# Kernel optimization log

Hardware: AMD Instinct MI355X
Metric: run time of the kernel (lower is better)

The kernel has to match this reference:

```python
import jax, jax.numpy as jnp
import numpy as np

B, L, D, H, M = 2, 4096, 1024, 16, 256
DH = D // H
EPS = 1e-6
LN_EPS = 1e-5


def setup_inputs() -> dict:
    key = jax.random.key(0)
    ks = jax.random.split(key, 6)
    inp = {
        "x": jax.random.normal(ks[0], (B, L, D), jnp.float32),
        "Wq": jax.random.normal(ks[1], (D, D), jnp.float32) * (D ** -0.5),
        "Wk": jax.random.normal(ks[2], (D, D), jnp.float32) * (D ** -0.5),
        "Wv": jax.random.normal(ks[3], (D, D), jnp.float32) * (D ** -0.5),
        "Wo": jax.random.normal(ks[4], (D, D), jnp.float32) * (D ** -0.5),
        "proj": jax.random.normal(ks[5], (H, M, DH), jnp.float32),
        "ln_g": jnp.ones((D,), jnp.float32),
        "ln_b": jnp.zeros((D,), jnp.float32),
        "scale_factor": 2,
    }
    return inp


def _heads(t, W):
    b, l, _ = t.shape
    return (t @ W).reshape(b, l, H, DH).transpose(0, 2, 1, 3)  # bhld


def _favor_features(u, proj):
    # u: [B,H,L,DH] already scaled by d_head**-0.25; proj: [H,M,DH]
    dash = jnp.einsum("bhld,hmd->bhlm", u, proj)
    diag = 0.5 * jnp.sum(u * u, axis=-1, keepdims=True)  # [B,H,L,1]
    stab = jnp.max(dash, axis=-1, keepdims=True)
    return jnp.exp(dash - diag - stab) * (M ** -0.5)  # [B,H,L,M]


def reference(x, Wq, Wk, Wv, Wo, proj, ln_g, ln_b, scale_factor):
    b, l, d = x.shape
    # nearest-neighbor upsample along sequence (F.interpolate default mode)
    up = jnp.repeat(x, scale_factor, axis=1)  # [B, L*s, D]

    scale = DH ** -0.25
    q = _heads(up, Wq) * scale   # [B,H,Lq,DH]
    k = _heads(x, Wk) * scale    # [B,H,L,DH]
    v = _heads(x, Wv)            # [B,H,L,DH]

    qf = _favor_features(q, proj)  # [B,H,Lq,M]
    kf = _favor_features(k, proj)  # [B,H,L,M]

    kv = jnp.einsum("bhlm,bhld->bhmd", kf, v)          # [B,H,M,DH]
    k_sum = jnp.sum(kf, axis=2)                          # [B,H,M]
    z = 1.0 / (jnp.einsum("bhlm,bhm->bhl", qf, k_sum) + EPS)
    attn = jnp.einsum("bhlm,bhmd->bhld", qf, kv) * z[..., None]

    lq = attn.shape[2]
    y = attn.transpose(0, 2, 1, 3).reshape(b, lq, d) @ Wo
    y = jax.nn.gelu(y, approximate=False)

    mu = jnp.mean(y, axis=-1, keepdims=True)
    var = jnp.mean((y - mu) ** 2, axis=-1, keepdims=True)
    return (y - mu) * jax.lax.rsqrt(var + LN_EPS) * ln_g + ln_b
```

## Files before the change

### kernel.cpp

```cpp
#include <hip/hip_runtime.h>

static constexpr int kB  = 2;
static constexpr int kL  = 4096;
static constexpr int kD  = 1024;
static constexpr int kH  = 16;
static constexpr int kDH = 64;
static constexpr int kM  = 256;
static constexpr int kN  = kB * kL;
static constexpr float kScale    = 0.35355339059327373f;
static constexpr float kInvSqrtM = 0.0625f;
static constexpr float kEps   = 1e-6f;
static constexpr float kLnEps = 1e-5f;

typedef __attribute__((ext_vector_type(8))) short short8;
typedef __attribute__((ext_vector_type(4))) float f32x4;

__device__ __forceinline__ float bf2f(unsigned short h) {
  union { unsigned int u; float f; } c;
  c.u = ((unsigned int)h) << 16;
  return c.f;
}
__device__ __forceinline__ unsigned short f2bf(float f) {
  union { float f; unsigned int u; } c;
  c.f = f;
  unsigned int u = c.u;
  u += 0x7fffu + ((u >> 16) & 1u);
  return (unsigned short)(u >> 16);
}

__device__ __forceinline__ void gload_lds16(const unsigned short* g,
                                            unsigned short* l) {
  __builtin_amdgcn_global_load_lds(
      (const __attribute__((address_space(1))) unsigned int*)g,
      (__attribute__((address_space(3))) unsigned int*)l, 16, 0, 0);
}

__device__ __forceinline__ void xcd_swizzle(int& bx, int& by) {
  const int nwg = gridDim.x * gridDim.y;
  const int bid = blockIdx.x + gridDim.x * blockIdx.y;
  const int cpx = nwg >> 3;
  const int sb  = (bid & 7) * cpx + (bid >> 3);
  bx = sb % gridDim.x;
  by = sb / gridDim.x;
}

__global__ __launch_bounds__(256) void cast_bf16_kernel(
    const float* __restrict__ in, unsigned short* __restrict__ out)
{
  const int i = blockIdx.x * 256 + threadIdx.x;
  float4 v = ((const float4*)in)[i];
  ushort4 o;
  o.x = f2bf(v.x); o.y = f2bf(v.y); o.z = f2bf(v.z); o.w = f2bf(v.w);
  ((ushort4*)out)[i] = o;
}

__global__ __launch_bounds__(256) void transpose_cast4_kernel(
    const float* __restrict__ W0, const float* __restrict__ W1,
    const float* __restrict__ W2, const float* __restrict__ W3,
    unsigned short* __restrict__ WqkvT, unsigned short* __restrict__ WoT)
{
  __shared__ float tile[32][33];
  const int z = blockIdx.z;
  const float* W = (z == 0) ? W0 : (z == 1) ? W1 : (z == 2) ? W2 : W3;
  unsigned short* WT = (z < 3) ? (WqkvT + (size_t)z * kD * kD) : WoT;
  const int n0 = blockIdx.x * 32, k0 = blockIdx.y * 32;
  const int t = threadIdx.x, kk = t >> 5, nn = t & 31;
#pragma unroll
  for (int i = 0; i < 4; ++i)
    tile[kk + i * 8][nn] = W[(size_t)(k0 + kk + i * 8) * kD + n0 + nn];
  __syncthreads();
#pragma unroll
  for (int i = 0; i < 4; ++i)
    WT[(size_t)(n0 + kk + i * 8) * kD + k0 + nn] = f2bf(tile[nn][kk + i * 8]);
}

__global__ __launch_bounds__(256) void gemm_qk_mfma(
    const unsigned short* __restrict__ A, const unsigned short* __restrict__ BT,
    unsigned short* __restrict__ Qb, unsigned short* __restrict__ Kb)
{
  __shared__ unsigned short As[128 * 32];
  __shared__ unsigned short Bs[128 * 32];
  const int tid = threadIdx.x, lane = tid & 63, w = tid >> 6;
  const int q = lane >> 4, c = lane & 15;
  const int wr = (w >> 1) * 64, wc = (w & 1) * 64;
  int bx, by; xcd_swizzle(bx, by);
  const int row0 = by * 128, col0 = bx * 128;
  const int lrow = lane >> 2, lcol = (lane & 3) * 8;

  f32x4 acc[4][4];
#pragma unroll
  for (int i = 0; i < 4; ++i)
#pragma unroll
    for (int j = 0; j < 4; ++j) acc[i][j] = (f32x4)0.f;

  for (int k0 = 0; k0 < kD; k0 += 32) {
#pragma unroll
    for (int i = 0; i < 2; ++i) {
      const int r0 = w * 32 + i * 16;
      gload_lds16(&A[(size_t)(row0 + r0 + lrow) * kD + k0 + lcol], &As[r0 * 32]);
      gload_lds16(&BT[(size_t)(col0 + r0 + lrow) * kD + k0 + lcol], &Bs[r0 * 32]);
    }
    __syncthreads();
    short8 av[4], bv[4];
#pragma unroll
    for (int i = 0; i < 4; ++i)
      av[i] = *(const short8*)&As[(wr + i * 16 + c) * 32 + q * 8];
#pragma unroll
    for (int j = 0; j < 4; ++j)
      bv[j] = *(const short8*)&Bs[(wc + j * 16 + c) * 32 + q * 8];
#pragma unroll
    for (int i = 0; i < 4; ++i)
#pragma unroll
      for (int j = 0; j < 4; ++j)
        acc[i][j] = __builtin_amdgcn_mfma_f32_16x16x32_bf16(
            av[i], bv[j], acc[i][j], 0, 0, 0);
    __syncthreads();
  }

  unsigned short* O = (col0 < 1024) ? Qb : Kb;
  const int cl0 = col0 & 1023;
#pragma unroll
  for (int i = 0; i < 4; ++i)
#pragma unroll
    for (int j = 0; j < 4; ++j)
#pragma unroll
      for (int r = 0; r < 4; ++r) {
        const int row = row0 + wr + i * 16 + q * 4 + r;
        const int col = cl0 + wc + j * 16 + c;
        O[(size_t)row * kD + col] = f2bf(kScale * acc[i][j][r]);
      }
}

__global__ __launch_bounds__(256) void gemm_vt_mfma(
    const unsigned short* __restrict__ A, const unsigned short* __restrict__ BT,
    unsigned short* __restrict__ VT)
{
  __shared__ unsigned short As[128 * 32];
  __shared__ unsigned short Bs[128 * 32];
  const int tid = threadIdx.x, lane = tid & 63, w = tid >> 6;
  const int q = lane >> 4, c = lane & 15;
  const int wr = (w >> 1) * 64, wc = (w & 1) * 64;
  int bx, by; xcd_swizzle(bx, by);
  const int row0 = bx * 128, col0 = by * 128;
  const int lrow = lane >> 2, lcol = (lane & 3) * 8;

  f32x4 acc[4][4];
#pragma unroll
  for (int i = 0; i < 4; ++i)
#pragma unroll
    for (int j = 0; j < 4; ++j) acc[i][j] = (f32x4)0.f;

  for (int k0 = 0; k0 < kD; k0 += 32) {
#pragma unroll
    for (int i = 0; i < 2; ++i) {
      const int r0 = w * 32 + i * 16;
      gload_lds16(&A[(size_t)(row0 + r0 + lrow) * kD + k0 + lcol], &As[r0 * 32]);
      gload_lds16(&BT[(size_t)(col0 + r0 + lrow) * kD + k0 + lcol], &Bs[r0 * 32]);
    }
    __syncthreads();
    short8 av[4], bv[4];
#pragma unroll
    for (int i = 0; i < 4; ++i)
      av[i] = *(const short8*)&As[(wr + i * 16 + c) * 32 + q * 8];
#pragma unroll
    for (int j = 0; j < 4; ++j)
      bv[j] = *(const short8*)&Bs[(wc + j * 16 + c) * 32 + q * 8];
#pragma unroll
    for (int i = 0; i < 4; ++i)
#pragma unroll
      for (int j = 0; j < 4; ++j)
        acc[i][j] = __builtin_amdgcn_mfma_f32_16x16x32_bf16(
            av[i], bv[j], acc[i][j], 0, 0, 0);
    __syncthreads();
  }

#pragma unroll
  for (int i = 0; i < 4; ++i)
#pragma unroll
    for (int j = 0; j < 4; ++j)
#pragma unroll
      for (int r = 0; r < 4; ++r) {
        const int row = row0 + wr + i * 16 + q * 4 + r;
        const int col = col0 + wc + j * 16 + c;
        const int bq = col >> 12, l = col & 4095;
        const int h = row >> 6, d = row & 63;
        VT[((size_t)((bq * 16 + h) * 64 + d)) * (size_t)kL + l] =
            f2bf(acc[i][j][r]);
      }
}

__global__ __launch_bounds__(256) void gemm_wo_mfma(
    const unsigned short* __restrict__ A, const unsigned short* __restrict__ BT,
    unsigned short* __restrict__ Yb)
{
  __shared__ unsigned short As[128 * 32];
  __shared__ unsigned short Bs[128 * 32];
  const int tid = threadIdx.x, lane = tid & 63, w = tid >> 6;
  const int q = lane >> 4, c = lane & 15;
  const int wr = (w >> 1) * 64, wc = (w & 1) * 64;
  int bx, by; xcd_swizzle(bx, by);
  const int row0 = by * 128, col0 = bx * 128;
  const int lrow = lane >> 2, lcol = (lane & 3) * 8;

  f32x4 acc[4][4];
#pragma unroll
  for (int i = 0; i < 4; ++i)
#pragma unroll
    for (int j = 0; j < 4; ++j) acc[i][j] = (f32x4)0.f;

  for (int k0 = 0; k0 < kD; k0 += 32) {
#pragma unroll
    for (int i = 0; i < 2; ++i) {
      const int r0 = w * 32 + i * 16;
      gload_lds16(&A[(size_t)(row0 + r0 + lrow) * kD + k0 + lcol], &As[r0 * 32]);
      gload_lds16(&BT[(size_t)(col0 + r0 + lrow) * kD + k0 + lcol], &Bs[r0 * 32]);
    }
    __syncthreads();
    short8 av[4], bv[4];
#pragma unroll
    for (int i = 0; i < 4; ++i)
      av[i] = *(const short8*)&As[(wr + i * 16 + c) * 32 + q * 8];
#pragma unroll
    for (int j = 0; j < 4; ++j)
      bv[j] = *(const short8*)&Bs[(wc + j * 16 + c) * 32 + q * 8];
#pragma unroll
    for (int i = 0; i < 4; ++i)
#pragma unroll
      for (int j = 0; j < 4; ++j)
        acc[i][j] = __builtin_amdgcn_mfma_f32_16x16x32_bf16(
            av[i], bv[j], acc[i][j], 0, 0, 0);
    __syncthreads();
  }

#pragma unroll
  for (int i = 0; i < 4; ++i)
#pragma unroll
    for (int j = 0; j < 4; ++j)
#pragma unroll
      for (int r = 0; r < 4; ++r) {
        const int row = row0 + wr + i * 16 + q * 4 + r;
        const int col = col0 + wc + j * 16 + c;
        Yb[(size_t)row * kD + col] = f2bf(acc[i][j][r]);
      }
}

__global__ __launch_bounds__(256) void favor_k_mfma(
    const unsigned short* __restrict__ U, const unsigned short* __restrict__ projb,
    unsigned short* __restrict__ F)
{
  __shared__ unsigned short Us[128 * 72];
  __shared__ unsigned short Ps[256 * 72];
  __shared__ float diagp[256];
  __shared__ float diag[128];
  unsigned short* Tbuf = Us;
  const int bh = blockIdx.x, b = bh >> 4, h = bh & 15;
  const int l0 = blockIdx.y * 128;
  const int tid = threadIdx.x, lane = tid & 63, w = tid >> 6;
  const int q = lane >> 4, c = lane & 15;
  const int wr = w * 32;

#pragma unroll
  for (int it = 0; it < 4; ++it) {
    int idx = it * 256 + tid;
    int row = idx >> 3, col8 = idx & 7;
    *(uint4*)&Us[row * 72 + col8 * 8] =
        *(const uint4*)&U[((size_t)(b * kL + l0 + row)) * kD + h * kDH + col8 * 8];
  }
#pragma unroll
  for (int it = 0; it < 8; ++it) {
    int idx = it * 256 + tid;
    int row = idx >> 3, col8 = idx & 7;
    *(uint4*)&Ps[row * 72 + col8 * 8] =
        *(const uint4*)&projb[((size_t)(h * kM + row)) * kDH + col8 * 8];
  }
  __syncthreads();

  {
    int row = tid & 127, half = tid >> 7;
    const unsigned short* ur = &Us[row * 72 + half * 32];
    float s = 0.f;
#pragma unroll
    for (int d8 = 0; d8 < 4; ++d8) {
      uint4 raw = *(const uint4*)&ur[d8 * 8];
      const unsigned short* us = (const unsigned short*)&raw;
#pragma unroll
      for (int j = 0; j < 8; ++j) { float v = bf2f(us[j]); s = fmaf(v, v, s); }
    }
    diagp[half * 128 + row] = s;
  }

  f32x4 acc[2][16];
#pragma unroll
  for (int i = 0; i < 2; ++i)
#pragma unroll
    for (int j = 0; j < 16; ++j) acc[i][j] = (f32x4)0.f;

#pragma unroll
  for (int ks = 0; ks < 2; ++ks) {
    short8 av[2];
#pragma unroll
    for (int i = 0; i < 2; ++i)
      av[i] = *(const short8*)&Us[(wr + i * 16 + c) * 72 + ks * 32 + q * 8];
#pragma unroll
    for (int jb = 0; jb < 2; ++jb) {
      short8 bv[8];
#pragma unroll
      for (int jl = 0; jl < 8; ++jl)
        bv[jl] = *(const short8*)&Ps[((jb * 8 + jl) * 16 + c) * 72 + ks * 32 + q * 8];
#pragma unroll
      for (int jl = 0; jl < 8; ++jl)
#pragma unroll
        for (int i = 0; i < 2; ++i)
          acc[i][jb * 8 + jl] = __builtin_amdgcn_mfma_f32_16x16x32_bf16(
              av[i], bv[jl], acc[i][jb * 8 + jl], 0, 0, 0);
    }
  }

  __syncthreads();
  if (tid < 128) diag[tid] = 0.5f * (diagp[tid] + diagp[128 + tid]);
  __syncthreads();

#pragma unroll
  for (int i = 0; i < 2; ++i)
#pragma unroll
    for (int r = 0; r < 4; ++r) {
      const int lrow = wr + i * 16 + q * 4 + r;
      float mx = -3.4e38f;
#pragma unroll
      for (int j = 0; j < 16; ++j) mx = fmaxf(mx, acc[i][j][r]);
      mx = fmaxf(mx, __shfl_xor(mx, 1, 64));
      mx = fmaxf(mx, __shfl_xor(mx, 2, 64));
      mx = fmaxf(mx, __shfl_xor(mx, 4, 64));
      mx = fmaxf(mx, __shfl_xor(mx, 8, 64));
      const float base = diag[lrow] + mx;
#pragma unroll
      for (int j = 0; j < 16; ++j)
        acc[i][j][r] = __expf(acc[i][j][r] - base) * kInvSqrtM;
    }

#pragma unroll
  for (int mc = 0; mc < 4; ++mc) {
    __syncthreads();
#pragma unroll
    for (int jl = 0; jl < 4; ++jl) {
      const int jj = mc * 4 + jl;
#pragma unroll
      for (int i = 0; i < 2; ++i) {
        ushort4 o;
        o.x = f2bf(acc[i][jj][0]); o.y = f2bf(acc[i][jj][1]);
        o.z = f2bf(acc[i][jj][2]); o.w = f2bf(acc[i][jj][3]);
        *(ushort4*)&Tbuf[(jl * 16 + c) * 136 + wr + i * 16 + q * 4] = o;
      }
    }
    __syncthreads();
#pragma unroll
    for (int it = 0; it < 4; ++it) {
      int idx = it * 256 + tid;
      int row = idx >> 4, col8 = idx & 15;
      *(uint4*)&F[((size_t)(bh * kM + mc * 64 + row)) * (size_t)kL +
                  l0 + col8 * 8] = *(const uint4*)&Tbuf[row * 136 + col8 * 8];
    }
  }
}

__global__ __launch_bounds__(256) void fused_qf_attn(
    const unsigned short* __restrict__ U, const unsigned short* __restrict__ projb,
    const unsigned short* __restrict__ KVT, unsigned short* __restrict__ ATTN)
{
  __shared__ unsigned short SA[27648];
  __shared__ float diagp[256];
  __shared__ float diag[128];
  unsigned short* Us  = SA;
  unsigned short* Ps  = SA + 9216;
  unsigned short* kvs = SA;
  unsigned short* qs  = SA + 21120;
  const int bh = blockIdx.x, b = bh >> 4, h = bh & 15;
  const int l0 = blockIdx.y * 128;
  const int tid = threadIdx.x, lane = tid & 63, w = tid >> 6;
  const int q = lane >> 4, c = lane & 15;
  const int wr = w * 32;

#pragma unroll
  for (int it = 0; it < 4; ++it) {
    int idx = it * 256 + tid;
    int row = idx >> 3, col8 = idx & 7;
    *(uint4*)&Us[row * 72 + col8 * 8] =
        *(const uint4*)&U[((size_t)(b * kL + l0 + row)) * kD + h * kDH + col8 * 8];
  }
#pragma unroll
  for (int it = 0; it < 8; ++it) {
    int idx = it * 256 + tid;
    int row = idx >> 3, col8 = idx & 7;
    *(uint4*)&Ps[row * 72 + col8 * 8] =
        *(const uint4*)&projb[((size_t)(h * kM + row)) * kDH + col8 * 8];
  }
  __syncthreads();

  {
    int row = tid & 127, half = tid >> 7;
    const unsigned short* ur = &Us[row * 72 + half * 32];
    float s = 0.f;
#pragma unroll
    for (int d8 = 0; d8 < 4; ++d8) {
      uint4 raw = *(const uint4*)&ur[d8 * 8];
      const unsigned short* us = (const unsigned short*)&raw;
#pragma unroll
      for (int j = 0; j < 8; ++j) { float v = bf2f(us[j]); s = fmaf(v, v, s); }
    }
    diagp[half * 128 + row] = s;
  }

  f32x4 acc[2][16];
#pragma unroll
  for (int i = 0; i < 2; ++i)
#pragma unroll
    for (int j = 0; j < 16; ++j) acc[i][j] = (f32x4)0.f;

#pragma unroll
  for (int ks = 0; ks < 2; ++ks) {
    short8 av[2];
#pragma unroll
    for (int i = 0; i < 2; ++i)
      av[i] = *(const short8*)&Us[(wr + i * 16 + c) * 72 + ks * 32 + q * 8];
#pragma unroll
    for (int jb = 0; jb < 2; ++jb) {
      short8 bv[8];
#pragma unroll
      for (int jl = 0; jl < 8; ++jl)
        bv[jl] = *(const short8*)&Ps[((jb * 8 + jl) * 16 + c) * 72 + ks * 32 + q * 8];
#pragma unroll
      for (int jl = 0; jl < 8; ++jl)
#pragma unroll
        for (int i = 0; i < 2; ++i)
          acc[i][jb * 8 + jl] = __builtin_amdgcn_mfma_f32_16x16x32_bf16(
              av[i], bv[jl], acc[i][jb * 8 + jl], 0, 0, 0);
    }
  }

  __syncthreads();
  if (tid < 128) diag[tid] = 0.5f * (diagp[tid] + diagp[128 + tid]);
#pragma unroll
  for (int it = 0; it < 10; ++it) {
    int idx = it * 256 + tid;
    int row = idx >> 5, col8 = (idx & 31) * 8;
    *(uint4*)&kvs[row * 264 + col8] =
        *(const uint4*)&KVT[(size_t)bh * (80 * kM) + row * kM + col8];
  }
  __syncthreads();

#pragma unroll
  for (int i = 0; i < 2; ++i)
#pragma unroll
    for (int r = 0; r < 4; ++r) {
      const int lrow = wr + i * 16 + q * 4 + r;
      float mx = -3.4e38f;
#pragma unroll
      for (int j = 0; j < 16; ++j) mx = fmaxf(mx, acc[i][j][r]);
      mx = fmaxf(mx, __shfl_xor(mx, 1, 64));
      mx = fmaxf(mx, __shfl_xor(mx, 2, 64));
      mx = fmaxf(mx, __shfl_xor(mx, 4, 64));
      mx = fmaxf(mx, __shfl_xor(mx, 8, 64));
      const float base = diag[lrow] + mx;
#pragma unroll
      for (int j = 0; j < 16; ++j)
        acc[i][j][r] = __expf(acc[i][j][r] - base) * kInvSqrtM;
    }

  f32x4 acc2[2][5];
#pragma unroll
  for (int i = 0; i < 2; ++i)
#pragma unroll
    for (int j = 0; j < 5; ++j) acc2[i][j] = (f32x4)0.f;

#pragma unroll
  for (int kk = 0; kk < 8; ++kk) {
#pragma unroll
    for (int i = 0; i < 2; ++i)
#pragma unroll
      for (int jj2 = 0; jj2 < 2; ++jj2) {
        const int jj = kk * 2 + jj2;
#pragma unroll
        for (int r = 0; r < 4; ++r)
          qs[(wr + i * 16 + q * 4 + r) * 40 + jj2 * 16 + c] =
              f2bf(acc[i][jj][r]);
      }
    __syncthreads();
    short8 bv2[5];
#pragma unroll
    for (int j = 0; j < 5; ++j)
      bv2[j] = *(const short8*)&kvs[(j * 16 + c) * 264 + kk * 32 + q * 8];
#pragma unroll
    for (int i = 0; i < 2; ++i) {
      short8 av2 = *(const short8*)&qs[(w * 32 + i * 16 + c) * 40 + q * 8];
#pragma unroll
      for (int j = 0; j < 5; ++j)
        acc2[i][j] = __builtin_amdgcn_mfma_f32_16x16x32_bf16(
            av2, bv2[j], acc2[i][j], 0, 0, 0);
    }
    __syncthreads();
  }

#pragma unroll
  for (int i = 0; i < 2; ++i)
#pragma unroll
    for (int r = 0; r < 4; ++r) {
      float den = __shfl(acc2[i][4][r], (lane & 48));
      float z = 1.f / (den + kEps);
      const int row = l0 + w * 32 + i * 16 + q * 4 + r;
      const size_t base = ((size_t)(b * kL + row)) * kD + h * kDH;
#pragma unroll
      for (int j = 0; j < 4; ++j)
        ATTN[base + j * 16 + c] = f2bf(acc2[i][j][r] * z);
    }
}

__global__ __launch_bounds__(256) void kv_mfma(
    const unsigned short* __restrict__ KFT, const unsigned short* __restrict__ VT,
    float* __restrict__ KVP, float* __restrict__ KSP)
{
  __shared__ unsigned short As[128 * 32];
  __shared__ unsigned short Bs[64 * 32];
  const int bh = blockIdx.x, mtile = blockIdx.y, split = blockIdx.z;
  const int tid = threadIdx.x, lane = tid & 63, w = tid >> 6;
  const int q = lane >> 4, c = lane & 15;
  const int l0 = split * 512;
  const unsigned short* Abase = KFT + ((size_t)(bh * kM + mtile * 128)) * kL + l0;
  const unsigned short* Bbase = VT + ((size_t)(bh * kDH)) * kL + l0;
  const int lrow = lane >> 2, lcol = (lane & 3) * 8;

  f32x4 acc[2][4];
#pragma unroll
  for (int i = 0; i < 2; ++i)
#pragma unroll
    for (int j = 0; j < 4; ++j) acc[i][j] = (f32x4)0.f;
  float ksr[2] = {0.f, 0.f};

  for (int k0 = 0; k0 < 512; k0 += 32) {
#pragma unroll
    for (int i = 0; i < 2; ++i) {
      const int r0 = w * 32 + i * 16;
      gload_lds16(&Abase[(size_t)(r0 + lrow) * kL + k0 + lcol], &As[r0 * 32]);
    }
    gload_lds16(&Bbase[(size_t)(w * 16 + lrow) * kL + k0 + lcol], &Bs[w * 16 * 32]);
    __syncthreads();
    short8 av[2], bv[4];
#pragma unroll
    for (int i = 0; i < 2; ++i) {
      av[i] = *(const short8*)&As[(w * 32 + i * 16 + c) * 32 + q * 8];
#pragma unroll
      for (int e = 0; e < 8; ++e) ksr[i] += bf2f((unsigned short)av[i][e]);
    }
#pragma unroll
    for (int j = 0; j < 4; ++j)
      bv[j] = *(const short8*)&Bs[(j * 16 + c) * 32 + q * 8];
#pragma unroll
    for (int i = 0; i < 2; ++i)
#pragma unroll
      for (int j = 0; j < 4; ++j)
        acc[i][j] = __builtin_amdgcn_mfma_f32_16x16x32_bf16(
            av[i], bv[j], acc[i][j], 0, 0, 0);
    __syncthreads();
  }

  const int blk = (bh * 2 + mtile) * 8 + split;
  float* op = KVP + (size_t)blk * (128 * 64);
#pragma unroll
  for (int i = 0; i < 2; ++i)
#pragma unroll
    for (int j = 0; j < 4; ++j)
#pragma unroll
      for (int r = 0; r < 4; ++r)
        op[(w * 32 + i * 16 + q * 4 + r) * 64 + j * 16 + c] = acc[i][j][r];

#pragma unroll
  for (int i = 0; i < 2; ++i) {
    float s = ksr[i];
    s += __shfl_xor(s, 16, 64);
    s += __shfl_xor(s, 32, 64);
    if (q == 0) KSP[blk * 128 + w * 32 + i * 16 + c] = s;
  }
}

__global__ __launch_bounds__(256) void kv_reduce_kernel(
    const float* __restrict__ KVP, const float* __restrict__ KSP,
    unsigned short* __restrict__ KVT)
{
  const int blk = blockIdx.x;
  const int bh = blk / 80, n = blk - bh * 80;
  const int t = threadIdx.x;
  const int mt = t >> 7, ml = t & 127;
  float s = 0.f;
  if (n < 64) {
#pragma unroll
    for (int sp = 0; sp < 8; ++sp)
      s += KVP[((size_t)((bh * 2 + mt) * 8 + sp)) * (128 * 64) + ml * 64 + n];
  } else if (n == 64) {
#pragma unroll
    for (int sp = 0; sp < 8; ++sp)
      s += KSP[((bh * 2 + mt) * 8 + sp) * 128 + ml];
  }
  KVT[(size_t)bh * (80 * kM) + n * kM + t] = f2bf(s);
}

__global__ __launch_bounds__(256) void gelu_ln_kernel(
    const unsigned short* __restrict__ Yb, const float* __restrict__ lng,
    const float* __restrict__ lnb, float* __restrict__ OUT)
{
  __shared__ float r1[4], r2[4];
  const int n = blockIdx.x;
  const int tid = threadIdx.x, lane = tid & 63, w = tid >> 6;

  ushort4 yv = ((const ushort4*)(Yb + (size_t)n * kD))[tid];
  float y0 = bf2f(yv.x), y1 = bf2f(yv.y), y2 = bf2f(yv.z), y3 = bf2f(yv.w);
  float g0 = 0.5f * y0 * (1.f + erff(y0 * 0.70710678118654752f));
  float g1 = 0.5f * y1 * (1.f + erff(y1 * 0.70710678118654752f));
  float g2 = 0.5f * y2 * (1.f + erff(y2 * 0.70710678118654752f));
  float g3 = 0.5f * y3 * (1.f + erff(y3 * 0.70710678118654752f));

  float s  = (g0 + g1) + (g2 + g3);
  float ss = (g0 * g0 + g1 * g1) + (g2 * g2 + g3 * g3);
#pragma unroll
  for (int off = 32; off; off >>= 1) {
    s  += __shfl_xor(s, off, 64);
    ss += __shfl_xor(ss, off, 64);
  }
  if (lane == 0) { r1[w] = s; r2[w] = ss; }
  __syncthreads();
  s  = (r1[0] + r1[1]) + (r1[2] + r1[3]);
  ss = (r2[0] + r2[1]) + (r2[2] + r2[3]);
  float mu  = s * (1.f / (float)kD);
  float var = ss * (1.f / (float)kD) - mu * mu;
  float inv = rsqrtf(var + kLnEps);

  float4 gg = ((const float4*)lng)[tid];
  float4 bb = ((const float4*)lnb)[tid];
  float4 o;
  o.x = (g0 - mu) * inv * gg.x + bb.x;
  o.y = (g1 - mu) * inv * gg.y + bb.y;
  o.z = (g2 - mu) * inv * gg.z + bb.z;
  o.w = (g3 - mu) * inv * gg.w + bb.w;

  const int b = n >> 12, l = n & 4095;
  const int cc = tid * 4;
  size_t base = ((size_t)(b * 8192 + 2 * l)) * kD + cc;
  *(float4*)(OUT + base)      = o;
  *(float4*)(OUT + base + kD) = o;
}

extern "C" void kernel_launch(void* const* d_in, const int* in_sizes, int n_in,
                              void* d_out, int out_size, void* d_ws, size_t ws_size,
                              hipStream_t stream)
{
  (void)in_sizes; (void)n_in; (void)out_size; (void)ws_size;
  const float* x    = (const float*)d_in[0];
  const float* Wq   = (const float*)d_in[1];
  const float* Wk   = (const float*)d_in[2];
  const float* Wv   = (const float*)d_in[3];
  const float* Wo   = (const float*)d_in[4];
  const float* proj = (const float*)d_in[5];
  const float* lng  = (const float*)d_in[6];
  const float* lnb  = (const float*)d_in[7];
  float* out = (float*)d_out;

  char* ws = (char*)d_ws;
  const size_t MB = 1024 * 1024;
  unsigned short* xb    = (unsigned short*)(ws);
  unsigned short* WqkvT = (unsigned short*)(ws + 16 * MB);
  unsigned short* WoT   = (unsigned short*)(ws + 22 * MB);
  unsigned short* Qb    = (unsigned short*)(ws + 24 * MB);
  unsigned short* Kb    = (unsigned short*)(ws + 40 * MB);
  unsigned short* VT    = (unsigned short*)(ws + 56 * MB);
  float* KVP            = (float*)(ws + 72 * MB);
  unsigned short* KFT   = (unsigned short*)(ws + 136 * MB);
  float* KSP            = (float*)(ws + 200 * MB);
  unsigned short* KVT   = (unsigned short*)(ws + 201 * MB);
  unsigned short* projb = (unsigned short*)(ws + 203 * MB);
  unsigned short* ATTN  = Kb;
  unsigned short* Yb    = (unsigned short*)(ws + 72 * MB);
  unsigned short* WvT   = WqkvT + (size_t)2 * kD * kD;

  cast_bf16_kernel<<<(kN * kD) / 1024, 256, 0, stream>>>(x, xb);
  cast_bf16_kernel<<<(kH * kM * kDH) / 1024, 256, 0, stream>>>(proj, projb);
  transpose_cast4_kernel<<<dim3(32, 32, 4), 256, 0, stream>>>(
      Wq, Wk, Wv, Wo, WqkvT, WoT);

  gemm_qk_mfma<<<dim3(16, 64), 256, 0, stream>>>(xb, WqkvT, Qb, Kb);
  gemm_vt_mfma<<<dim3(8, 64), 256, 0, stream>>>(WvT, xb, VT);

  favor_k_mfma<<<dim3(32, 32), 256, 0, stream>>>(Kb, projb, KFT);
  kv_mfma<<<dim3(32, 2, 8), 256, 0, stream>>>(KFT, VT, KVP, KSP);
  kv_reduce_kernel<<<32 * 80, 256, 0, stream>>>(KVP, KSP, KVT);

  fused_qf_attn<<<dim3(32, 32), 256, 0, stream>>>(Qb, projb, KVT, ATTN);

  gemm_wo_mfma<<<dim3(8, 64), 256, 0, stream>>>(ATTN, WoT, Yb);

  gelu_ln_kernel<<<kN, 256, 0, stream>>>(Yb, lng, lnb, out);
}
```

Before: 336.3 us.

## Compute q normalizer from ksum directly and halve projection LDS buffer

In the fused q-feature attention kernel, the projection matrix is now staged into shared memory in two 128-row halves instead of all 256 rows at once. The denominator is computed as a per-row dot product of the fp32 features with a small ksum vector held in LDS, replacing the fifth padded MFMA column tile. Together these shrink the kernel's shared-memory footprint, likely to raise occupancy, and drop one MFMA tile per step. The cost is an extra barrier and reload between halves, plus scalar FMAs and shuffles for the denominator.

Result: no change. 341.3 us (+1.5%).

```diff
diff --git a/kernel.cpp b/kernel.cpp
--- a/kernel.cpp
+++ b/kernel.cpp
@@ -367,13 +367,14 @@
     const unsigned short* __restrict__ U, const unsigned short* __restrict__ projb,
     const unsigned short* __restrict__ KVT, unsigned short* __restrict__ ATTN)
 {
-  __shared__ unsigned short SA[27648];
+  __shared__ unsigned short SA[22016];
   __shared__ float diagp[256];
   __shared__ float diag[128];
+  __shared__ unsigned short ksumS[256];
   unsigned short* Us  = SA;
-  unsigned short* Ps  = SA + 9216;
+  unsigned short* Ps2 = SA + 9216;
   unsigned short* kvs = SA;
-  unsigned short* qs  = SA + 21120;
+  unsigned short* qs  = SA + 16896;
   const int bh = blockIdx.x, b = bh >> 4, h = bh & 15;
   const int l0 = blockIdx.y * 128;
   const int tid = threadIdx.x, lane = tid & 63, w = tid >> 6;
@@ -388,10 +389,10 @@
         *(const uint4*)&U[((size_t)(b * kL + l0 + row)) * kD + h * kDH + col8 * 8];
   }
 #pragma unroll
-  for (int it = 0; it < 8; ++it) {
+  for (int it = 0; it < 4; ++it) {
     int idx = it * 256 + tid;
     int row = idx >> 3, col8 = idx & 7;
-    *(uint4*)&Ps[row * 72 + col8 * 8] =
+    *(uint4*)&Ps2[row * 72 + col8 * 8] =
         *(const uint4*)&projb[((size_t)(h * kM + row)) * kDH + col8 * 8];
   }
   __syncthreads();
@@ -417,35 +418,49 @@
     for (int j = 0; j < 16; ++j) acc[i][j] = (f32x4)0.f;
 
 #pragma unroll
-  for (int ks = 0; ks < 2; ++ks) {
-    short8 av[2];
-#pragma unroll
-    for (int i = 0; i < 2; ++i)
-      av[i] = *(const short8*)&Us[(wr + i * 16 + c) * 72 + ks * 32 + q * 8];
-#pragma unroll
-    for (int jb = 0; jb < 2; ++jb) {
+  for (int half = 0; half < 2; ++half) {
+    if (half == 1) {
+      __syncthreads();
+#pragma unroll
+      for (int it = 0; it < 4; ++it) {
+        int idx = it * 256 + tid;
+        int row = idx >> 3, col8 = idx & 7;
+        *(uint4*)&Ps2[row * 72 + col8 * 8] =
+            *(const uint4*)&projb[((size_t)(h * kM + 128 + row)) * kDH + col8 * 8];
+      }
+      __syncthreads();
+    }
+#pragma unroll
+    for (int ks = 0; ks < 2; ++ks) {
+      short8 av[2];
+#pragma unroll
+      for (int i = 0; i < 2; ++i)
+        av[i] = *(const short8*)&Us[(wr + i * 16 + c) * 72 + ks * 32 + q * 8];
       short8 bv[8];
 #pragma unroll
       for (int jl = 0; jl < 8; ++jl)
-        bv[jl] = *(const short8*)&Ps[((jb * 8 + jl) * 16 + c) * 72 + ks * 32 + q * 8];
+        bv[jl] = *(const short8*)&Ps2[(jl * 16 + c) * 72 + ks * 32 + q * 8];
 #pragma unroll
       for (int jl = 0; jl < 8; ++jl)
 #pragma unroll
         for (int i = 0; i < 2; ++i)
-          acc[i][jb * 8 + jl] = __builtin_amdgcn_mfma_f32_16x16x32_bf16(
-              av[i], bv[jl], acc[i][jb * 8 + jl], 0, 0, 0);
+          acc[i][half * 8 + jl] = __builtin_amdgcn_mfma_f32_16x16x32_bf16(
+              av[i], bv[jl], acc[i][half * 8 + jl], 0, 0, 0);
     }
   }
 
   __syncthreads();
   if (tid < 128) diag[tid] = 0.5f * (diagp[tid] + diagp[128 + tid]);
 #pragma unroll
-  for (int it = 0; it < 10; ++it) {
+  for (int it = 0; it < 8; ++it) {
     int idx = it * 256 + tid;
     int row = idx >> 5, col8 = (idx & 31) * 8;
     *(uint4*)&kvs[row * 264 + col8] =
         *(const uint4*)&KVT[(size_t)bh * (80 * kM) + row * kM + col8];
   }
+  if (tid < 32)
+    *(uint4*)&ksumS[tid * 8] =
+        *(const uint4*)&KVT[(size_t)bh * (80 * kM) + 64 * kM + tid * 8];
   __syncthreads();
 
 #pragma unroll
@@ -466,11 +481,27 @@
         acc[i][j][r] = __expf(acc[i][j][r] - base) * kInvSqrtM;
     }
 
-  f32x4 acc2[2][5];
-#pragma unroll
-  for (int i = 0; i < 2; ++i)
-#pragma unroll
-    for (int j = 0; j < 5; ++j) acc2[i][j] = (f32x4)0.f;
+  float z_[2][4];
+#pragma unroll
+  for (int i = 0; i < 2; ++i)
+#pragma unroll
+    for (int r = 0; r < 4; ++r) {
+      float d = 0.f;
+#pragma unroll
+      for (int j = 0; j < 16; ++j)
+        d = fmaf(acc[i][j][r], bf2f(ksumS[j * 16 + c]), d);
+      d += __shfl_xor(d, 1, 64);
+      d += __shfl_xor(d, 2, 64);
+      d += __shfl_xor(d, 4, 64);
+      d += __shfl_xor(d, 8, 64);
+      z_[i][r] = 1.f / (d + kEps);
+    }
+
+  f32x4 acc2[2][4];
+#pragma unroll
+  for (int i = 0; i < 2; ++i)
+#pragma unroll
+    for (int j = 0; j < 4; ++j) acc2[i][j] = (f32x4)0.f;
 
 #pragma unroll
   for (int kk = 0; kk < 8; ++kk) {
@@ -485,15 +516,15 @@
               f2bf(acc[i][jj][r]);
       }
     __syncthreads();
-    short8 bv2[5];
-#pragma unroll
-    for (int j = 0; j < 5; ++j)
+    short8 bv2[4];
+#pragma unroll
+    for (int j = 0; j < 4; ++j)
       bv2[j] = *(const short8*)&kvs[(j * 16 + c) * 264 + kk * 32 + q * 8];
 #pragma unroll
     for (int i = 0; i < 2; ++i) {
       short8 av2 = *(const short8*)&qs[(w * 32 + i * 16 + c) * 40 + q * 8];
 #pragma unroll
-      for (int j = 0; j < 5; ++j)
+      for (int j = 0; j < 4; ++j)
         acc2[i][j] = __builtin_amdgcn_mfma_f32_16x16x32_bf16(
             av2, bv2[j], acc2[i][j], 0, 0, 0);
     }
@@ -504,13 +535,11 @@
   for (int i = 0; i < 2; ++i)
 #pragma unroll
     for (int r = 0; r < 4; ++r) {
-      float den = __shfl(acc2[i][4][r], (lane & 48));
-      float z = 1.f / (den + kEps);
       const int row = l0 + w * 32 + i * 16 + q * 4 + r;
       const size_t base = ((size_t)(b * kL + row)) * kD + h * kDH;
 #pragma unroll
       for (int j = 0; j < 4; ++j)
-        ATTN[base + j * 16 + c] = f2bf(acc2[i][j][r] * z);
+        ATTN[base + j * 16 + c] = f2bf(acc2[i][j][r] * z_[i][r]);
     }
 }
 
```
